# Kernel optimization log

Measured on AMD Instinct MI355X. Metric: run time of the kernel, lower is better.

Reference implementation:

```python
import jax, jax.numpy as jnp
import numpy as np

N_NODES = 50000
N_EDGES = 800000
D_IN = 64
D_OUT = 64

def setup_inputs() -> dict:
    key = jax.random.key(0)
    k1, k2, k3, k4 = jax.random.split(key, 4)
    x = jax.random.normal(k1, (N_NODES, D_IN), dtype=jnp.float32)
    # Linear(in, out, bias=False): weight shape [out, in], Kaiming-uniform-ish scale
    bound = 1.0 / np.sqrt(D_IN)
    W = jax.random.uniform(k2, (D_OUT, D_IN), dtype=jnp.float32, minval=-bound, maxval=bound)
    src = jax.random.randint(k3, (N_EDGES,), 0, N_NODES, dtype=jnp.int32)
    dst = jax.random.randint(k4, (N_EDGES,), 0, N_NODES, dtype=jnp.int32)
    return {"x": x, "W": W, "src": src, "dst": dst}

def reference(x, W, src, dst):
    # update_all(copy_src, sum): for each edge (s, d), add x[s] into node d
    agg = jax.ops.segment_sum(x[src], dst, num_segments=N_NODES)  # [N, D_IN]
    # linear1 (bias=False); dropout is identity at inference
    h = jnp.einsum('nd,od->no', agg, W)  # [N, D_OUT]
    h = jax.nn.relu(h)
    # is_normalize=False -> skip L2 normalize; residual adds input node features
    return h + x
```

## Files before the change

### kernel.cpp

```cpp
#include <hip/hip_runtime.h>

#define D 64
#define NCHUNK 256
#define HISTB NCHUNK
#define GEMMB 1024
#define CAP 48

__device__ __forceinline__ float bflo(unsigned u) { return __uint_as_float(u << 16); }
__device__ __forceinline__ float bfhi(unsigned u) { return __uint_as_float(u & 0xffff0000u); }
__device__ __forceinline__ unsigned short f2bf(float f) {
    unsigned b = __float_as_uint(f);
    return (unsigned short)((b + 0x7fffu + ((b >> 16) & 1u)) >> 16);
}

__global__ __launch_bounds__(256) void hist_gemm_kernel(
    const float* __restrict__ x, const float* __restrict__ W,
    const int* __restrict__ dst, unsigned int* __restrict__ bh32,
    unsigned short* __restrict__ ybf, int n_nodes, int ne) {
    __shared__ unsigned int lds[12544];
    const int tid = threadIdx.x;
    const int nw = (n_nodes + 3) >> 2;
    if (blockIdx.x < HISTB) {
        const int c = blockIdx.x;
        const int csz = (ne + NCHUNK - 1) / NCHUNK;
        const int e0 = c * csz, e1 = min(e0 + csz, ne);
        for (int i = tid; i < nw; i += 256) lds[i] = 0;
        __syncthreads();
        for (int e = e0 + tid; e < e1; e += 256) {
            const int d = dst[e];
            atomicAdd(&lds[d >> 2], 1u << ((d & 3) * 8));
        }
        __syncthreads();
        unsigned int* bh = bh32 + (size_t)c * nw;
        for (int i = tid; i < nw; i += 256) bh[i] = lds[i];
    } else {
        float* Wt = (float*)lds;
        float* As = Wt + 64 * 65;
        for (int i = tid; i < 4096; i += 256) {
            const int o = i >> 6, k = i & 63;
            Wt[k * 65 + o] = W[i];
        }
        const int w = tid >> 6, o = tid & 63;
        const float4* x4 = (const float4*)x;
        const int ngrp = (n_nodes + 15) >> 4;
        for (int grp = blockIdx.x - HISTB; grp < ngrp; grp += GEMMB) {
            const int base = grp * 16;
            __syncthreads();
            const int idx = base * 16 + tid;
            if (idx < n_nodes * 16) ((float4*)As)[tid] = x4[idx];
            __syncthreads();
            const float* a0 = &As[(w * 4 + 0) * 64];
            const float* a1 = &As[(w * 4 + 1) * 64];
            const float* a2 = &As[(w * 4 + 2) * 64];
            const float* a3 = &As[(w * 4 + 3) * 64];
            float h0 = 0.f, h1 = 0.f, h2 = 0.f, h3 = 0.f;
#pragma unroll
            for (int k = 0; k < 64; ++k) {
                const float wv = Wt[k * 65 + o];
                h0 = fmaf(a0[k], wv, h0);
                h1 = fmaf(a1[k], wv, h1);
                h2 = fmaf(a2[k], wv, h2);
                h3 = fmaf(a3[k], wv, h3);
            }
            const int n0 = base + w * 4;
            if (n0 + 3 < n_nodes) {
                ybf[(size_t)(n0 + 0) * D + o] = f2bf(h0);
                ybf[(size_t)(n0 + 1) * D + o] = f2bf(h1);
                ybf[(size_t)(n0 + 2) * D + o] = f2bf(h2);
                ybf[(size_t)(n0 + 3) * D + o] = f2bf(h3);
            } else {
                if (n0 + 0 < n_nodes) ybf[(size_t)(n0 + 0) * D + o] = f2bf(h0);
                if (n0 + 1 < n_nodes) ybf[(size_t)(n0 + 1) * D + o] = f2bf(h1);
                if (n0 + 2 < n_nodes) ybf[(size_t)(n0 + 2) * D + o] = f2bf(h2);
                if (n0 + 3 < n_nodes) ybf[(size_t)(n0 + 3) * D + o] = f2bf(h3);
            }
        }
    }
}

__global__ void colscan_kernel(unsigned char* __restrict__ bh8,
                               int* __restrict__ counts, int n_nodes) {
    const int d = blockIdx.x * 256 + threadIdx.x;
    if (d >= n_nodes) return;
    const size_t npad4 = (size_t)((n_nodes + 3) >> 2) * 4;
    int acc = 0;
    for (int c0 = 0; c0 < NCHUNK; c0 += 8) {
        unsigned char v[8];
#pragma unroll
        for (int k = 0; k < 8; ++k) v[k] = bh8[(size_t)(c0 + k) * npad4 + d];
#pragma unroll
        for (int k = 0; k < 8; ++k) {
            bh8[(size_t)(c0 + k) * npad4 + d] = (unsigned char)acc;
            acc += v[k];
        }
    }
    counts[d] = acc;
}

__global__ __launch_bounds__(256) void place_kernel(
    const int* __restrict__ src, const int* __restrict__ dst,
    const unsigned int* __restrict__ bh32, int* __restrict__ esrc,
    int n_nodes, int ne) {
    __shared__ unsigned int lw[12544];
    const int c = blockIdx.x;
    const int csz = (ne + NCHUNK - 1) / NCHUNK;
    const int e0 = c * csz, e1 = min(e0 + csz, ne);
    const int nw = (n_nodes + 3) >> 2;
    const unsigned int* bh = bh32 + (size_t)c * nw;
    for (int i = threadIdx.x; i < nw; i += 256) lw[i] = bh[i];
    __syncthreads();
    for (int e = e0 + threadIdx.x; e < e1; e += 256) {
        const int d = dst[e];
        const unsigned old = atomicAdd(&lw[d >> 2], 1u << ((d & 3) * 8));
        const int slot = (old >> ((d & 3) * 8)) & 0xff;
        if (slot < CAP) esrc[d * CAP + slot] = src[e];
    }
}

__global__ void gather_kernel(const int* __restrict__ counts, const int* __restrict__ esrc,
                              const unsigned short* __restrict__ ybf,
                              const float* __restrict__ x, float* __restrict__ out,
                              int n_nodes) {
    const int tid = threadIdx.x;
    const int w = tid >> 6, lane = tid & 63;
    const int g = lane >> 3, m = lane & 7;
    const uint4* Y4 = (const uint4*)ybf;
    const float4* x4 = (const float4*)x;
    float4* out4 = (float4*)out;
    const int nWaves = gridDim.x * 4;

    int n = blockIdx.x * 4 + w;
    int c = 0, s_all = 0;
    if (n < n_nodes) {
        c = min(counts[n], CAP);
        s_all = (lane < c) ? esrc[n * CAP + lane] : 0;
    }
    while (n < n_nodes) {
        const int n2 = n + nWaves;
        int c2 = 0, s2 = 0;
        if (n2 < n_nodes) {
            c2 = min(counts[n2], CAP);
            s2 = (lane < c2) ? esrc[n2 * CAP + lane] : 0;
        }
        float acc[8] = {0.f, 0.f, 0.f, 0.f, 0.f, 0.f, 0.f, 0.f};
        for (int j = 0; j < c; j += 8) {
            const int e = j + g;
            const int s = __shfl(s_all, e);
            if (e < c) {
                const uint4 v = Y4[(size_t)s * 8 + m];
                acc[0] += bflo(v.x); acc[1] += bfhi(v.x);
                acc[2] += bflo(v.y); acc[3] += bfhi(v.y);
                acc[4] += bflo(v.z); acc[5] += bfhi(v.z);
                acc[6] += bflo(v.w); acc[7] += bfhi(v.w);
            }
        }
#pragma unroll
        for (int k = 0; k < 8; ++k) {
            acc[k] += __shfl_xor(acc[k], 8);
            acc[k] += __shfl_xor(acc[k], 16);
            acc[k] += __shfl_xor(acc[k], 32);
        }
        if (lane < 8) {
            const float4 xa = x4[(size_t)n * 16 + lane * 2];
            const float4 xb = x4[(size_t)n * 16 + lane * 2 + 1];
            float4 oa, ob;
            oa.x = fmaxf(acc[0], 0.f) + xa.x;
            oa.y = fmaxf(acc[1], 0.f) + xa.y;
            oa.z = fmaxf(acc[2], 0.f) + xa.z;
            oa.w = fmaxf(acc[3], 0.f) + xa.w;
            ob.x = fmaxf(acc[4], 0.f) + xb.x;
            ob.y = fmaxf(acc[5], 0.f) + xb.y;
            ob.z = fmaxf(acc[6], 0.f) + xb.z;
            ob.w = fmaxf(acc[7], 0.f) + xb.w;
            out4[(size_t)n * 16 + lane * 2] = oa;
            out4[(size_t)n * 16 + lane * 2 + 1] = ob;
        }
        n = n2; c = c2; s_all = s2;
    }
}

extern "C" void kernel_launch(void* const* d_in, const int* in_sizes, int n_in,
                              void* d_out, int out_size, void* d_ws, size_t ws_size,
                              hipStream_t stream) {
    const float* x = (const float*)d_in[0];
    const float* W = (const float*)d_in[1];
    const int* src = (const int*)d_in[2];
    const int* dst = (const int*)d_in[3];
    float* out = (float*)d_out;

    const int n_nodes = in_sizes[0] / D;
    const int n_edges = in_sizes[2];
    const int nw = (n_nodes + 3) >> 2;

    unsigned int* bh32 = (unsigned int*)d_ws;
    int* counts = (int*)(bh32 + (size_t)NCHUNK * nw);
    int* esrc = counts + n_nodes;
    unsigned short* ybf = (unsigned short*)(esrc + (size_t)n_nodes * CAP);

    hist_gemm_kernel<<<HISTB + GEMMB, 256, 0, stream>>>(x, W, dst, bh32, ybf,
                                                        n_nodes, n_edges);
    colscan_kernel<<<(n_nodes + 255) / 256, 256, 0, stream>>>((unsigned char*)bh32,
                                                              counts, n_nodes);
    place_kernel<<<HISTB, 256, 0, stream>>>(src, dst, bh32, esrc, n_nodes, n_edges);
    gather_kernel<<<2048, 256, 0, stream>>>(counts, esrc, ybf, x, out, n_nodes);
}
```

Measured before the change: 141.5 us.

## Move GEMM blocks from histogram kernel into column-scan kernel

The dense x·Wᵀ bf16 GEMM now shares a launch with the column-scan instead of the histogram pass. The histogram kernel runs alone with its 50 KB LDS footprint, and the GEMM blocks in the colscan launch need only about 20 KB of LDS. This is meant to balance work across launches and let the GEMM overlap the latency-bound column scan. The cost is that the histogram pass no longer hides the GEMM, so the new pairing may not overlap better.

```diff
diff --git a/kernel.cpp b/kernel.cpp
--- a/kernel.cpp
+++ b/kernel.cpp
@@ -2,7 +2,6 @@
 
 #define D 64
 #define NCHUNK 256
-#define HISTB NCHUNK
 #define GEMMB 1024
 #define CAP 48
 
@@ -13,28 +12,49 @@
     return (unsigned short)((b + 0x7fffu + ((b >> 16) & 1u)) >> 16);
 }
 
-__global__ __launch_bounds__(256) void hist_gemm_kernel(
-    const float* __restrict__ x, const float* __restrict__ W,
-    const int* __restrict__ dst, unsigned int* __restrict__ bh32,
-    unsigned short* __restrict__ ybf, int n_nodes, int ne) {
+__global__ __launch_bounds__(256) void hist_kernel(
+    const int* __restrict__ dst, unsigned int* __restrict__ bh32, int n_nodes, int ne) {
     __shared__ unsigned int lds[12544];
     const int tid = threadIdx.x;
     const int nw = (n_nodes + 3) >> 2;
-    if (blockIdx.x < HISTB) {
-        const int c = blockIdx.x;
-        const int csz = (ne + NCHUNK - 1) / NCHUNK;
-        const int e0 = c * csz, e1 = min(e0 + csz, ne);
-        for (int i = tid; i < nw; i += 256) lds[i] = 0;
-        __syncthreads();
-        for (int e = e0 + tid; e < e1; e += 256) {
-            const int d = dst[e];
-            atomicAdd(&lds[d >> 2], 1u << ((d & 3) * 8));
-        }
-        __syncthreads();
-        unsigned int* bh = bh32 + (size_t)c * nw;
-        for (int i = tid; i < nw; i += 256) bh[i] = lds[i];
+    const int c = blockIdx.x;
+    const int csz = (ne + NCHUNK - 1) / NCHUNK;
+    const int e0 = c * csz, e1 = min(e0 + csz, ne);
+    for (int i = tid; i < nw; i += 256) lds[i] = 0;
+    __syncthreads();
+    for (int e = e0 + tid; e < e1; e += 256) {
+        const int d = dst[e];
+        atomicAdd(&lds[d >> 2], 1u << ((d & 3) * 8));
+    }
+    __syncthreads();
+    unsigned int* bh = bh32 + (size_t)c * nw;
+    for (int i = tid; i < nw; i += 256) bh[i] = lds[i];
+}
+
+__global__ __launch_bounds__(256) void colscan_gemm_kernel(
+    const float* __restrict__ x, const float* __restrict__ W,
+    unsigned char* __restrict__ bh8, int* __restrict__ counts,
+    unsigned short* __restrict__ ybf, int n_nodes, int ne, int csb) {
+    __shared__ float lds[5184];
+    const int tid = threadIdx.x;
+    if ((int)blockIdx.x < csb) {
+        const int d = blockIdx.x * 256 + tid;
+        if (d >= n_nodes) return;
+        const size_t npad4 = (size_t)((n_nodes + 3) >> 2) * 4;
+        int acc = 0;
+        for (int c0 = 0; c0 < NCHUNK; c0 += 8) {
+            unsigned char v[8];
+#pragma unroll
+            for (int k = 0; k < 8; ++k) v[k] = bh8[(size_t)(c0 + k) * npad4 + d];
+#pragma unroll
+            for (int k = 0; k < 8; ++k) {
+                bh8[(size_t)(c0 + k) * npad4 + d] = (unsigned char)acc;
+                acc += v[k];
+            }
+        }
+        counts[d] = acc;
     } else {
-        float* Wt = (float*)lds;
+        float* Wt = lds;
         float* As = Wt + 64 * 65;
         for (int i = tid; i < 4096; i += 256) {
             const int o = i >> 6, k = i & 63;
@@ -43,7 +63,7 @@
         const int w = tid >> 6, o = tid & 63;
         const float4* x4 = (const float4*)x;
         const int ngrp = (n_nodes + 15) >> 4;
-        for (int grp = blockIdx.x - HISTB; grp < ngrp; grp += GEMMB) {
+        for (int grp = blockIdx.x - csb; grp < ngrp; grp += GEMMB) {
             const int base = grp * 16;
             __syncthreads();
             const int idx = base * 16 + tid;
@@ -76,25 +96,6 @@
             }
         }
     }
-}
-
-__global__ void colscan_kernel(unsigned char* __restrict__ bh8,
-                               int* __restrict__ counts, int n_nodes) {
-    const int d = blockIdx.x * 256 + threadIdx.x;
-    if (d >= n_nodes) return;
-    const size_t npad4 = (size_t)((n_nodes + 3) >> 2) * 4;
-    int acc = 0;
-    for (int c0 = 0; c0 < NCHUNK; c0 += 8) {
-        unsigned char v[8];
-#pragma unroll
-        for (int k = 0; k < 8; ++k) v[k] = bh8[(size_t)(c0 + k) * npad4 + d];
-#pragma unroll
-        for (int k = 0; k < 8; ++k) {
-            bh8[(size_t)(c0 + k) * npad4 + d] = (unsigned char)acc;
-            acc += v[k];
-        }
-    }
-    counts[d] = acc;
 }
 
 __global__ __launch_bounds__(256) void place_kernel(
@@ -197,10 +198,11 @@
     int* esrc = counts + n_nodes;
     unsigned short* ybf = (unsigned short*)(esrc + (size_t)n_nodes * CAP);
 
-    hist_gemm_kernel<<<HISTB + GEMMB, 256, 0, stream>>>(x, W, dst, bh32, ybf,
-                                                        n_nodes, n_edges);
-    colscan_kernel<<<(n_nodes + 255) / 256, 256, 0, stream>>>((unsigned char*)bh32,
-                                                              counts, n_nodes);
-    place_kernel<<<HISTB, 256, 0, stream>>>(src, dst, bh32, esrc, n_nodes, n_edges);
+    const int csb = (n_nodes + 255) / 256;
+
+    hist_kernel<<<NCHUNK, 256, 0, stream>>>(dst, bh32, n_nodes, n_edges);
+    colscan_gemm_kernel<<<csb + GEMMB, 256, 0, stream>>>(
+        x, W, (unsigned char*)bh32, counts, ybf, n_nodes, n_edges, csb);
+    place_kernel<<<NCHUNK, 256, 0, stream>>>(src, dst, bh32, esrc, n_nodes, n_edges);
     gather_kernel<<<2048, 256, 0, stream>>>(counts, esrc, ybf, x, out, n_nodes);
 }
```

After: 136.0 us. 3.9% less time.
